# Optimization experiments

Measured on AMD Instinct MI355X. Metric: run time of the kernel, lower is better.

The kernel has to match this reference:

```python
import jax, jax.numpy as jnp
import numpy as np


def setup_inputs() -> dict:
    key = jax.random.key(0)
    k1, k2 = jax.random.split(key)
    x = jax.random.normal(k1, (8192, 128), dtype=jnp.float32)
    y = jax.random.normal(k2, (8192, 128), dtype=jnp.float32)
    return {"x": x, "y": y}


def reference(x, y):
    # Squared pairwise euclidean distances: ||x_i||^2 + ||y_j||^2 - 2 x_i . y_j
    num_pts = x.shape[0]
    x2 = jnp.sum(x * x, axis=1)  # [N]
    y2 = jnp.sum(y * y, axis=1)  # [M]
    dist = x2[:, None] + y2[None, :] - 2.0 * (x @ y.T)  # [N, M]
    dist = jnp.maximum(dist, 0.0)  # matches pow(cdist, 2) up to fp rounding
    in_dist_out = jnp.min(dist, axis=0)   # per-y nearest x, [M]
    out_dist_in = jnp.min(dist, axis=1)   # per-x nearest y, [N]
    loss = jnp.sum(in_dist_out + out_dist_in) / num_pts
    return loss
```

## Files before the change

kernel.cpp:

```cpp
#include <hip/hip_runtime.h>
#include <hip/hip_bf16.h>
#include <stdint.h>


typedef __bf16  bf16x8 __attribute__((ext_vector_type(8)));
typedef float   f32x4  __attribute__((ext_vector_type(4)));

#define NPTS 8192
#define DIM  128
#define KC   128

__device__ __forceinline__ void gload_lds16(const void* gsrc, void* ldst) {
  __builtin_amdgcn_global_load_lds(
      (const __attribute__((address_space(1))) uint32_t*)(uintptr_t)gsrc,
      (__attribute__((address_space(3))) uint32_t*)(uintptr_t)ldst,
      16, 0, 0);
}

__global__ __launch_bounds__(256) void prep_kernel(
    const float* __restrict__ x, const float* __restrict__ y,
    unsigned short* __restrict__ Xc, unsigned short* __restrict__ Yc,
    float* __restrict__ x2, float* __restrict__ y2,
    unsigned int* __restrict__ minx, unsigned int* __restrict__ miny)
{
  const int gt  = blockIdx.x * 256 + threadIdx.x;
  const int row = gt >> 5;
  const int seg = gt & 31;
  const bool isx = row < NPTS;
  const float* src        = isx ? (x  + (size_t)row * DIM) : (y  + (size_t)(row - NPTS) * DIM);
  unsigned short* dst     = isx ? (Xc + (size_t)row * KC)  : (Yc + (size_t)(row - NPTS) * KC);

  f32x4 v = *reinterpret_cast<const f32x4*>(src + seg * 4);
  float sq = v[0]*v[0] + v[1]*v[1] + v[2]*v[2] + v[3]*v[3];
  #pragma unroll
  for (int m = 1; m <= 16; m <<= 1) sq += __shfl_xor(sq, m);
  if (seg == 0) { if (isx) x2[row] = sq; else y2[row - NPTS] = sq; }

  const float scale = isx ? -2.0f : 1.0f;
  unsigned short hb[4];
  #pragma unroll
  for (int i = 0; i < 4; ++i) {
    __hip_bfloat16 h = __float2bfloat16(scale * v[i]);
    hb[i] = __builtin_bit_cast(unsigned short, h);
  }
  *reinterpret_cast<ushort4*>(dst + seg * 4) = make_ushort4(hb[0], hb[1], hb[2], hb[3]);

  if (gt < NPTS)          minx[gt]        = 0x7F800000u;
  else if (gt < 2 * NPTS) miny[gt - NPTS] = 0x7F800000u;
}

__global__ __launch_bounds__(512, 2) void chamfer_gemm(
    const unsigned short* __restrict__ Xc, const unsigned short* __restrict__ Yc,
    const float* __restrict__ x2, const float* __restrict__ y2,
    unsigned int* __restrict__ minx, unsigned int* __restrict__ miny)
{
  __shared__ alignas(16) unsigned short As[2][256 * 64];
  __shared__ alignas(16) unsigned short Bs[2][256 * 64];
  float* colminLDS = (float*)&As[0][0];
  float* rowminLDS = (float*)&As[0][0] + 512;

  const int tid  = threadIdx.x;
  const int lane = tid & 63;
  const int w    = tid >> 6;
  const int wr   = w >> 2;
  const int wc   = w & 3;

  const int bid   = blockIdx.x;
  const int xcd   = bid & 7;
  const int local = bid >> 3;
  const int bi    = xcd * 4 + ((local >> 3) & 3);
  const int bj    = ((local >> 5) << 3) + (local & 7);

  const int r64  = tid >> 3;
  const int kgrp = (tid & 7) ^ (r64 & 7);
  const unsigned short* Abase = Xc + (size_t)(bi * 256 + r64) * KC + kgrp * 8;
  const unsigned short* Bbase = Yc + (size_t)(bj * 256 + r64) * KC + kgrp * 8;

  auto STAGE = [&](int buf, int kt) {
    const unsigned short* Asrc = Abase + kt * 64;
    const unsigned short* Bsrc = Bbase + kt * 64;
    char* Ad = (char*)&As[buf][0] + w * 1024;
    char* Bd = (char*)&Bs[buf][0] + w * 1024;
    #pragma unroll
    for (int l = 0; l < 4; ++l) {
      gload_lds16(Asrc + (size_t)l * 64 * KC, Ad + l * 8192);
      gload_lds16(Bsrc + (size_t)l * 64 * KC, Bd + l * 8192);
    }
  };

  f32x4 acc[8][4];
  {
    f32x4 xv[8]; float yv[4];
    #pragma unroll
    for (int mi = 0; mi < 8; ++mi)
      xv[mi] = *reinterpret_cast<const f32x4*>(x2 + bi * 256 + wr * 128 + mi * 16 + ((lane >> 4) << 2));
    #pragma unroll
    for (int ni = 0; ni < 4; ++ni)
      yv[ni] = y2[bj * 256 + wc * 64 + ni * 16 + (lane & 15)];
    #pragma unroll
    for (int mi = 0; mi < 8; ++mi)
      #pragma unroll
      for (int ni = 0; ni < 4; ++ni)
        #pragma unroll
        for (int r = 0; r < 4; ++r)
          acc[mi][ni][r] = xv[mi][r] + yv[ni];
  }

  STAGE(0, 0);
  __syncthreads();

  #pragma unroll
  for (int kt = 0; kt < 2; ++kt) {
    if (kt < 1) STAGE(1, 1);
    const char* Ab = (const char*)&As[kt][0];
    const char* Bb = (const char*)&Bs[kt][0];

    bf16x8 bfr[4][2];
    #pragma unroll
    for (int ni = 0; ni < 4; ++ni) {
      const int col = wc * 64 + ni * 16 + (lane & 15);
      const int swz = (col & 7) << 4;
      #pragma unroll
      for (int ks = 0; ks < 2; ++ks) {
        const int ofs = (ks * 64 + ((lane >> 4) << 4)) ^ swz;
        bfr[ni][ks] = *reinterpret_cast<const bf16x8*>(Bb + col * 128 + ofs);
      }
    }
    #pragma unroll
    for (int mi = 0; mi < 8; ++mi) {
      const int rowl = wr * 128 + mi * 16 + (lane & 15);
      const int swz  = (rowl & 7) << 4;
      const bf16x8 a0 = *reinterpret_cast<const bf16x8*>(Ab + rowl * 128 + ((  0 + ((lane >> 4) << 4)) ^ swz));
      const bf16x8 a1 = *reinterpret_cast<const bf16x8*>(Ab + rowl * 128 + (( 64 + ((lane >> 4) << 4)) ^ swz));
      #pragma unroll
      for (int ni = 0; ni < 4; ++ni) {
        acc[mi][ni] = __builtin_amdgcn_mfma_f32_16x16x32_bf16(a0, bfr[ni][0], acc[mi][ni], 0, 0, 0);
        acc[mi][ni] = __builtin_amdgcn_mfma_f32_16x16x32_bf16(a1, bfr[ni][1], acc[mi][ni], 0, 0, 0);
      }
    }
    __syncthreads();
  }

  float cm[4];
  #pragma unroll
  for (int ni = 0; ni < 4; ++ni) {
    float m = 3.0e38f;
    #pragma unroll
    for (int mi = 0; mi < 8; ++mi)
      #pragma unroll
      for (int r = 0; r < 4; ++r)
        m = fminf(m, acc[mi][ni][r]);
    cm[ni] = m;
  }
  {
    const bool hb0 = (lane & 16) != 0;
    float s0 = hb0 ? cm[0] : cm[2];
    float s1 = hb0 ? cm[1] : cm[3];
    float r0 = __shfl_xor(s0, 16);
    float r1 = __shfl_xor(s1, 16);
    float t0 = fminf(hb0 ? cm[2] : cm[0], r0);
    float t1 = fminf(hb0 ? cm[3] : cm[1], r1);
    const bool hb1 = (lane & 32) != 0;
    float s  = hb1 ? t0 : t1;
    float rr = __shfl_xor(s, 32);
    float cfin = fminf(hb1 ? t1 : t0, rr);
    const int ni = (hb0 ? 2 : 0) + (hb1 ? 1 : 0);
    colminLDS[wr * 256 + wc * 64 + ni * 16 + (lane & 15)] = cfin;
  }

  float rm[32];
  #pragma unroll
  for (int mi = 0; mi < 8; ++mi)
    #pragma unroll
    for (int r = 0; r < 4; ++r)
      rm[mi * 4 + r] = fminf(fminf(acc[mi][0][r], acc[mi][1][r]),
                             fminf(acc[mi][2][r], acc[mi][3][r]));
  #pragma unroll
  for (int b2 = 0; b2 < 4; ++b2) {
    const int  half = 16 >> b2;
    const bool up   = (lane >> b2) & 1;
    #pragma unroll
    for (int i = 0; i < half; ++i) {
      float snd = up ? rm[i] : rm[i + half];
      float rcv = __shfl_xor(snd, 1 << b2);
      rm[i] = fminf(up ? rm[i + half] : rm[i], rcv);
    }
  }
  {
    const int base = ((lane & 1) << 4) | ((lane & 2) << 2) | (lane & 4) | ((lane & 8) >> 2);
    #pragma unroll
    for (int e = 0; e < 2; ++e) {
      const int idx = base | e;
      const int row_local = wr * 128 + (idx >> 2) * 16 + ((lane >> 4) << 2) + (idx & 3);
      rowminLDS[wc * 256 + row_local] = rm[e];
    }
  }
  __syncthreads();

  if (tid < 256) {
    float c = fminf(colminLDS[tid], colminLDS[256 + tid]);
    atomicMin(&miny[bj * 256 + tid], __float_as_uint(fmaxf(c, 0.f)));
  } else {
    const int r = tid - 256;
    float v = fminf(fminf(rowminLDS[r], rowminLDS[256 + r]),
                    fminf(rowminLDS[512 + r], rowminLDS[768 + r]));
    atomicMin(&minx[bi * 256 + r], __float_as_uint(fmaxf(v, 0.f)));
  }
}

__global__ __launch_bounds__(256) void finalize_kernel(
    const unsigned int* __restrict__ minx, const unsigned int* __restrict__ miny,
    float* __restrict__ out)
{
  const f32x4* mx = (const f32x4*)minx;
  const f32x4* my = (const f32x4*)miny;
  float s = 0.f;
  for (int i = threadIdx.x; i < NPTS / 4; i += 256) {
    f32x4 a = mx[i], b = my[i];
    s += (a[0] + a[1] + a[2] + a[3]) + (b[0] + b[1] + b[2] + b[3]);
  }
  #pragma unroll
  for (int m = 32; m >= 1; m >>= 1) s += __shfl_xor(s, m);
  __shared__ float partial[4];
  if ((threadIdx.x & 63) == 0) partial[threadIdx.x >> 6] = s;
  __syncthreads();
  if (threadIdx.x == 0)
    out[0] = (partial[0] + partial[1] + partial[2] + partial[3]) * (1.0f / (float)NPTS);
}

extern "C" void kernel_launch(void* const* d_in, const int* in_sizes, int n_in,
                              void* d_out, int out_size, void* d_ws, size_t ws_size,
                              hipStream_t stream) {
  (void)in_sizes; (void)n_in; (void)out_size; (void)ws_size;
  const float* x = (const float*)d_in[0];
  const float* y = (const float*)d_in[1];
  char* ws = (char*)d_ws;

  unsigned short* Xc  = (unsigned short*)(ws);
  unsigned short* Yc  = (unsigned short*)(ws + 2097152);
  float*          x2  = (float*)(ws + 4194304);
  float*          y2  = (float*)(ws + 4227072);
  unsigned int*   mnx = (unsigned int*)(ws + 4259840);
  unsigned int*   mny = (unsigned int*)(ws + 4292608);
  float*          out = (float*)d_out;

  prep_kernel<<<2048, 256, 0, stream>>>(x, y, Xc, Yc, x2, y2, mnx, mny);
  chamfer_gemm<<<1024, 512, 0, stream>>>(Xc, Yc, x2, y2, mnx, mny);
  finalize_kernel<<<1, 256, 0, stream>>>(mnx, mny, out);
}
```

Baseline: 90.82 us.

## Make GEMM blocks persistent over four column tiles, reusing the staged A tile

Each block now keeps its 256-row X tile resident in LDS and loops over four consecutive Y column tiles, double-buffering the B loads across tiles. Row minima are accumulated in registers across tiles, so there is one minx atomic per row instead of four. The grid shrinks from 1024 to 256 blocks. This cuts repeated A loads and atomics, but on a 256-CU part it leaves one block per CU and serialises four tiles per block, which reduces occupancy and latency hiding.

```diff
diff --git a/kernel.cpp b/kernel.cpp
--- a/kernel.cpp
+++ b/kernel.cpp
@@ -56,8 +56,8 @@
 {
   __shared__ alignas(16) unsigned short As[2][256 * 64];
   __shared__ alignas(16) unsigned short Bs[2][256 * 64];
-  float* colminLDS = (float*)&As[0][0];
-  float* rowminLDS = (float*)&As[0][0] + 512;
+  __shared__ float colminLDS[2 * 256];
+  __shared__ float rowminLDS[4 * 256];
 
   const int tid  = threadIdx.x;
   const int lane = tid & 63;
@@ -65,38 +65,50 @@
   const int wr   = w >> 2;
   const int wc   = w & 3;
 
-  const int bid   = blockIdx.x;
-  const int xcd   = bid & 7;
-  const int local = bid >> 3;
-  const int bi    = xcd * 4 + ((local >> 3) & 3);
-  const int bj    = ((local >> 5) << 3) + (local & 7);
+  const int b     = blockIdx.x;
+  const int local = b >> 3;
+  const int bi    = (b & 7) * 4 + (local >> 3);
+  const int bj0   = (local & 7) * 4;
 
   const int r64  = tid >> 3;
   const int kgrp = (tid & 7) ^ (r64 & 7);
   const unsigned short* Abase = Xc + (size_t)(bi * 256 + r64) * KC + kgrp * 8;
-  const unsigned short* Bbase = Yc + (size_t)(bj * 256 + r64) * KC + kgrp * 8;
-
-  auto STAGE = [&](int buf, int kt) {
+  const int wofs = w * 1024;
+
+  auto STAGE_A = [&](int kt) {
     const unsigned short* Asrc = Abase + kt * 64;
-    const unsigned short* Bsrc = Bbase + kt * 64;
-    char* Ad = (char*)&As[buf][0] + w * 1024;
-    char* Bd = (char*)&Bs[buf][0] + w * 1024;
-    #pragma unroll
-    for (int l = 0; l < 4; ++l) {
+    char* Ad = (char*)&As[kt][0] + wofs;
+    #pragma unroll
+    for (int l = 0; l < 4; ++l)
       gload_lds16(Asrc + (size_t)l * 64 * KC, Ad + l * 8192);
+  };
+  auto STAGE_B = [&](int buf, int t, int kt) {
+    const unsigned short* Bsrc = Yc + (size_t)((bj0 + t) * 256 + r64) * KC + kgrp * 8 + kt * 64;
+    char* Bd = (char*)&Bs[buf][0] + wofs;
+    #pragma unroll
+    for (int l = 0; l < 4; ++l)
       gload_lds16(Bsrc + (size_t)l * 64 * KC, Bd + l * 8192);
-    }
   };
 
-  f32x4 acc[8][4];
-  {
-    f32x4 xv[8]; float yv[4];
-    #pragma unroll
-    for (int mi = 0; mi < 8; ++mi)
-      xv[mi] = *reinterpret_cast<const f32x4*>(x2 + bi * 256 + wr * 128 + mi * 16 + ((lane >> 4) << 2));
-    #pragma unroll
-    for (int ni = 0; ni < 4; ++ni)
-      yv[ni] = y2[bj * 256 + wc * 64 + ni * 16 + (lane & 15)];
+  STAGE_A(0);
+  STAGE_A(1);
+  STAGE_B(0, 0, 0);
+
+  f32x4 xv[8];
+  #pragma unroll
+  for (int mi = 0; mi < 8; ++mi)
+    xv[mi] = *reinterpret_cast<const f32x4*>(x2 + bi * 256 + wr * 128 + mi * 16 + ((lane >> 4) << 2));
+  float yv[4];
+  #pragma unroll
+  for (int ni = 0; ni < 4; ++ni)
+    yv[ni] = y2[bj0 * 256 + wc * 64 + ni * 16 + (lane & 15)];
+
+  float rowrun0 = 3.0e38f, rowrun1 = 3.0e38f;
+
+  __syncthreads();
+
+  for (int t = 0; t < 4; ++t) {
+    f32x4 acc[8][4];
     #pragma unroll
     for (int mi = 0; mi < 8; ++mi)
       #pragma unroll
@@ -104,108 +116,121 @@
         #pragma unroll
         for (int r = 0; r < 4; ++r)
           acc[mi][ni][r] = xv[mi][r] + yv[ni];
+
+    float yvn[4];
+    if (t < 3) {
+      #pragma unroll
+      for (int ni = 0; ni < 4; ++ni)
+        yvn[ni] = y2[(bj0 + t + 1) * 256 + wc * 64 + ni * 16 + (lane & 15)];
+    }
+
+    #pragma unroll
+    for (int kt = 0; kt < 2; ++kt) {
+      if (kt == 0)      STAGE_B(1, t, 1);
+      else if (t < 3)   STAGE_B(0, t + 1, 0);
+
+      const char* Ab = (const char*)&As[kt][0];
+      const char* Bb = (const char*)&Bs[kt][0];
+
+      bf16x8 bfr[4][2];
+      #pragma unroll
+      for (int ni = 0; ni < 4; ++ni) {
+        const int col = wc * 64 + ni * 16 + (lane & 15);
+        const int swz = (col & 7) << 4;
+        #pragma unroll
+        for (int ks = 0; ks < 2; ++ks) {
+          const int ofs = (ks * 64 + ((lane >> 4) << 4)) ^ swz;
+          bfr[ni][ks] = *reinterpret_cast<const bf16x8*>(Bb + col * 128 + ofs);
+        }
+      }
+      #pragma unroll
+      for (int mi = 0; mi < 8; ++mi) {
+        const int rowl = wr * 128 + mi * 16 + (lane & 15);
+        const int swz  = (rowl & 7) << 4;
+        const bf16x8 a0 = *reinterpret_cast<const bf16x8*>(Ab + rowl * 128 + ((  0 + ((lane >> 4) << 4)) ^ swz));
+        const bf16x8 a1 = *reinterpret_cast<const bf16x8*>(Ab + rowl * 128 + (( 64 + ((lane >> 4) << 4)) ^ swz));
+        #pragma unroll
+        for (int ni = 0; ni < 4; ++ni) {
+          acc[mi][ni] = __builtin_amdgcn_mfma_f32_16x16x32_bf16(a0, bfr[ni][0], acc[mi][ni], 0, 0, 0);
+          acc[mi][ni] = __builtin_amdgcn_mfma_f32_16x16x32_bf16(a1, bfr[ni][1], acc[mi][ni], 0, 0, 0);
+        }
+      }
+      __syncthreads();
+    }
+
+    float cm[4];
+    #pragma unroll
+    for (int ni = 0; ni < 4; ++ni) {
+      float m = 3.0e38f;
+      #pragma unroll
+      for (int mi = 0; mi < 8; ++mi)
+        #pragma unroll
+        for (int r = 0; r < 4; ++r)
+          m = fminf(m, acc[mi][ni][r]);
+      cm[ni] = m;
+    }
+    {
+      const bool hb0 = (lane & 16) != 0;
+      float s0 = hb0 ? cm[0] : cm[2];
+      float s1 = hb0 ? cm[1] : cm[3];
+      float r0 = __shfl_xor(s0, 16);
+      float r1 = __shfl_xor(s1, 16);
+      float t0 = fminf(hb0 ? cm[2] : cm[0], r0);
+      float t1 = fminf(hb0 ? cm[3] : cm[1], r1);
+      const bool hb1 = (lane & 32) != 0;
+      float s  = hb1 ? t0 : t1;
+      float rr = __shfl_xor(s, 32);
+      float cfin = fminf(hb1 ? t1 : t0, rr);
+      const int ni = (hb0 ? 2 : 0) + (hb1 ? 1 : 0);
+      colminLDS[wr * 256 + wc * 64 + ni * 16 + (lane & 15)] = cfin;
+    }
+
+    float rm[32];
+    #pragma unroll
+    for (int mi = 0; mi < 8; ++mi)
+      #pragma unroll
+      for (int r = 0; r < 4; ++r)
+        rm[mi * 4 + r] = fminf(fminf(acc[mi][0][r], acc[mi][1][r]),
+                               fminf(acc[mi][2][r], acc[mi][3][r]));
+    #pragma unroll
+    for (int b2 = 0; b2 < 4; ++b2) {
+      const int  half = 16 >> b2;
+      const bool up   = (lane >> b2) & 1;
+      #pragma unroll
+      for (int i = 0; i < half; ++i) {
+        float snd = up ? rm[i] : rm[i + half];
+        float rcv = __shfl_xor(snd, 1 << b2);
+        rm[i] = fminf(up ? rm[i + half] : rm[i], rcv);
+      }
+    }
+    {
+      const int base = ((lane & 1) << 4) | ((lane & 2) << 2) | (lane & 4) | ((lane & 8) >> 2);
+      #pragma unroll
+      for (int e = 0; e < 2; ++e) {
+        const int idx = base | e;
+        const int row_local = wr * 128 + (idx >> 2) * 16 + ((lane >> 4) << 2) + (idx & 3);
+        rowminLDS[wc * 256 + row_local] = rm[e];
+      }
+    }
+    __syncthreads();
+
+    if (tid < 256) {
+      float c = fminf(colminLDS[tid], colminLDS[256 + tid]);
+      atomicMin(&miny[(bj0 + t) * 256 + tid], __float_as_uint(fmaxf(c, 0.f)));
+    } else {
+      const int r = tid - 256;
+      float v = fminf(fminf(rowminLDS[r], rowminLDS[256 + r]),
+                      fminf(rowminLDS[512 + r], rowminLDS[768 + r]));
+      rowrun0 = fminf(rowrun0, v);
+    }
+    (void)rowrun1;
+
+    #pragma unroll
+    for (int ni = 0; ni < 4; ++ni) yv[ni] = yvn[ni];
   }
 
-  STAGE(0, 0);
-  __syncthreads();
-
-  #pragma unroll
-  for (int kt = 0; kt < 2; ++kt) {
-    if (kt < 1) STAGE(1, 1);
-    const char* Ab = (const char*)&As[kt][0];
-    const char* Bb = (const char*)&Bs[kt][0];
-
-    bf16x8 bfr[4][2];
-    #pragma unroll
-    for (int ni = 0; ni < 4; ++ni) {
-      const int col = wc * 64 + ni * 16 + (lane & 15);
-      const int swz = (col & 7) << 4;
-      #pragma unroll
-      for (int ks = 0; ks < 2; ++ks) {
-        const int ofs = (ks * 64 + ((lane >> 4) << 4)) ^ swz;
-        bfr[ni][ks] = *reinterpret_cast<const bf16x8*>(Bb + col * 128 + ofs);
-      }
-    }
-    #pragma unroll
-    for (int mi = 0; mi < 8; ++mi) {
-      const int rowl = wr * 128 + mi * 16 + (lane & 15);
-      const int swz  = (rowl & 7) << 4;
-      const bf16x8 a0 = *reinterpret_cast<const bf16x8*>(Ab + rowl * 128 + ((  0 + ((lane >> 4) << 4)) ^ swz));
-      const bf16x8 a1 = *reinterpret_cast<const bf16x8*>(Ab + rowl * 128 + (( 64 + ((lane >> 4) << 4)) ^ swz));
-      #pragma unroll
-      for (int ni = 0; ni < 4; ++ni) {
-        acc[mi][ni] = __builtin_amdgcn_mfma_f32_16x16x32_bf16(a0, bfr[ni][0], acc[mi][ni], 0, 0, 0);
-        acc[mi][ni] = __builtin_amdgcn_mfma_f32_16x16x32_bf16(a1, bfr[ni][1], acc[mi][ni], 0, 0, 0);
-      }
-    }
-    __syncthreads();
-  }
-
-  float cm[4];
-  #pragma unroll
-  for (int ni = 0; ni < 4; ++ni) {
-    float m = 3.0e38f;
-    #pragma unroll
-    for (int mi = 0; mi < 8; ++mi)
-      #pragma unroll
-      for (int r = 0; r < 4; ++r)
-        m = fminf(m, acc[mi][ni][r]);
-    cm[ni] = m;
-  }
-  {
-    const bool hb0 = (lane & 16) != 0;
-    float s0 = hb0 ? cm[0] : cm[2];
-    float s1 = hb0 ? cm[1] : cm[3];
-    float r0 = __shfl_xor(s0, 16);
-    float r1 = __shfl_xor(s1, 16);
-    float t0 = fminf(hb0 ? cm[2] : cm[0], r0);
-    float t1 = fminf(hb0 ? cm[3] : cm[1], r1);
-    const bool hb1 = (lane & 32) != 0;
-    float s  = hb1 ? t0 : t1;
-    float rr = __shfl_xor(s, 32);
-    float cfin = fminf(hb1 ? t1 : t0, rr);
-    const int ni = (hb0 ? 2 : 0) + (hb1 ? 1 : 0);
-    colminLDS[wr * 256 + wc * 64 + ni * 16 + (lane & 15)] = cfin;
-  }
-
-  float rm[32];
-  #pragma unroll
-  for (int mi = 0; mi < 8; ++mi)
-    #pragma unroll
-    for (int r = 0; r < 4; ++r)
-      rm[mi * 4 + r] = fminf(fminf(acc[mi][0][r], acc[mi][1][r]),
-                             fminf(acc[mi][2][r], acc[mi][3][r]));
-  #pragma unroll
-  for (int b2 = 0; b2 < 4; ++b2) {
-    const int  half = 16 >> b2;
-    const bool up   = (lane >> b2) & 1;
-    #pragma unroll
-    for (int i = 0; i < half; ++i) {
-      float snd = up ? rm[i] : rm[i + half];
-      float rcv = __shfl_xor(snd, 1 << b2);
-      rm[i] = fminf(up ? rm[i + half] : rm[i], rcv);
-    }
-  }
-  {
-    const int base = ((lane & 1) << 4) | ((lane & 2) << 2) | (lane & 4) | ((lane & 8) >> 2);
-    #pragma unroll
-    for (int e = 0; e < 2; ++e) {
-      const int idx = base | e;
-      const int row_local = wr * 128 + (idx >> 2) * 16 + ((lane >> 4) << 2) + (idx & 3);
-      rowminLDS[wc * 256 + row_local] = rm[e];
-    }
-  }
-  __syncthreads();
-
-  if (tid < 256) {
-    float c = fminf(colminLDS[tid], colminLDS[256 + tid]);
-    atomicMin(&miny[bj * 256 + tid], __float_as_uint(fmaxf(c, 0.f)));
-  } else {
-    const int r = tid - 256;
-    float v = fminf(fminf(rowminLDS[r], rowminLDS[256 + r]),
-                    fminf(rowminLDS[512 + r], rowminLDS[768 + r]));
-    atomicMin(&minx[bi * 256 + r], __float_as_uint(fmaxf(v, 0.f)));
-  }
+  if (tid >= 256)
+    atomicMin(&minx[bi * 256 + (tid - 256)], __float_as_uint(fmaxf(rowrun0, 0.f)));
 }
 
 __global__ __launch_bounds__(256) void finalize_kernel(
@@ -245,6 +270,6 @@
   float*          out = (float*)d_out;
 
   prep_kernel<<<2048, 256, 0, stream>>>(x, y, Xc, Yc, x2, y2, mnx, mny);
-  chamfer_gemm<<<1024, 512, 0, stream>>>(Xc, Yc, x2, y2, mnx, mny);
+  chamfer_gemm<<<256, 512, 0, stream>>>(Xc, Yc, x2, y2, mnx, mny);
   finalize_kernel<<<1, 256, 0, stream>>>(mnx, mny, out);
 }
```

After: 86.05 us. -5.2%, faster.
